# Optimization experiments

Measured on AMD Instinct MI355X. Metric: run time of the kernel, lower is better.

## Reference

```python
import jax, jax.numpy as jnp
import numpy as np

N = 50000          # num_nodes
IN_CH = 128
H = 32             # hidden_channels
D = 2              # stalk dimension d (= final_d, add_lp=add_hp=False)
LAYERS = 4
EU = 400000        # undirected edges
E = 2 * EU         # directed edges (both orientations)
OUT = 32


def setup_inputs() -> dict:
    key = jax.random.key(0)
    ks = jax.random.split(key, 12)
    # undirected random graph; directed edge list holds both orientations so that
    # the reverse of directed edge e is e + EU (mod E)
    u = jax.random.randint(ks[0], (EU,), 0, N)
    v = jax.random.randint(ks[1], (EU,), 0, N)
    edge_index = jnp.stack([jnp.concatenate([u, v]), jnp.concatenate([v, u])]).astype(jnp.int64)
    x = jax.random.normal(ks[2], (N, IN_CH), dtype=jnp.float32)
    W1 = jax.random.normal(ks[3], (H * D, IN_CH), dtype=jnp.float32) / np.sqrt(IN_CH)
    b1 = jax.random.normal(ks[4], (H * D,), dtype=jnp.float32) * 0.01
    W_sheaf = jax.random.normal(ks[5], (LAYERS, D, 2 * D * H), dtype=jnp.float32) / np.sqrt(2 * D * H)
    # lin_left initialised to identity in the module; keep near-identity
    W_left = jnp.tile(jnp.eye(D, dtype=jnp.float32), (LAYERS, 1, 1)) \
        + 0.01 * jax.random.normal(ks[6], (LAYERS, D, D), dtype=jnp.float32)
    W_right = jax.random.normal(ks[7], (LAYERS, H, H), dtype=jnp.float32) / np.sqrt(H)
    eps = jnp.zeros((LAYERS, D, 1), dtype=jnp.float32) + 0.01 * jax.random.normal(ks[8], (LAYERS, D, 1), dtype=jnp.float32)
    W2 = jax.random.normal(ks[9], (OUT, D * H), dtype=jnp.float32) / np.sqrt(D * H)
    b2 = jax.random.normal(ks[10], (OUT,), dtype=jnp.float32) * 0.01
    return {"x": x, "edge_index": edge_index, "W1": W1, "b1": b1, "W_sheaf": W_sheaf,
            "W_left": W_left, "W_right": W_right, "eps": eps, "W2": W2, "b2": b2}


def reference(x, edge_index, W1, b1, W_sheaf, W_left, W_right, eps, W2, b2):
    # eval mode: dropouts are no-ops; diagnostic energies/eigsh omitted (no effect on output)
    n = x.shape[0]
    d = W_left.shape[-1]
    h = W_right.shape[-1]
    src, dst = edge_index[0], edge_index[1]
    e = src.shape[0]
    rev = (jnp.arange(e) + e // 2) % e  # reverse directed edge

    x = jax.nn.elu(x @ W1.T + b1)      # [N, d*h]
    x = x.reshape(n * d, h)
    x0 = x

    for l in range(W_left.shape[0]):
        # --- sheaf learner: tanh(Linear([x_i || x_j])), diag maps F: [E, d] ---
        xn = x.reshape(n, d * h)
        feat = jnp.concatenate([xn[src], xn[dst]], axis=-1)   # [E, 2dh]
        F = jnp.tanh(feat @ W_sheaf[l].T)                     # [E, d]
        Fr = F[rev]
        # --- diag sheaf Laplacian (normalised, augmented: D_hat = D + I) ---
        Dg = jax.ops.segment_sum(F * F, src, num_segments=n)  # [N, d] diagonal blocks
        dinv = jax.lax.rsqrt(Dg + 1.0)
        diagw = Dg * dinv * dinv                              # [N, d]
        offw = -F * Fr * dinv[src] * dinv[dst]                # [E, d]
        # --- left weights: view x^T as [h, N, d], mix stalk dim ---
        xt = x.T.reshape(h, n, d) @ W_left[l].T
        x = xt.reshape(h, n * d).T
        # --- right weights ---
        x = x @ W_right[l].T
        # --- spmm: y = L x ---
        x3 = x.reshape(n, d, h)
        y = diagw[:, :, None] * x3 \
            + jax.ops.segment_sum(offw[:, :, None] * x3[dst], src, num_segments=n)
        x = jax.nn.elu(y.reshape(n * d, h))
        # --- epsilon-gated residual ---
        coeff = jnp.tile(1.0 + jnp.tanh(eps[l]), (n, 1))      # [N*d, 1]
        x0 = coeff * x0 - x
        x = x0

    return x.reshape(n, d * h) @ W2.T + b2
```

## Files before the change

### kernel.cpp

```cpp
#include <hip/hip_runtime.h>
#include <math.h>

#define INCH 128
#define DH 64
#define H  32
#define D  2
#define LAYERS 4
#define OUTC 32

typedef __fp16 half4 __attribute__((ext_vector_type(4)));
typedef float  f32x4 __attribute__((ext_vector_type(4)));

__device__ __forceinline__ float eluf(float v) { return v > 0.f ? v : expm1f(v); }

__device__ __forceinline__ float ftanh(float x) {
    float xc = fminf(9.0f, fmaxf(-9.0f, x));
    float e2 = __builtin_amdgcn_exp2f(xc * 2.885390081777927f);
    return (e2 - 1.0f) * __builtin_amdgcn_rcpf(e2 + 1.0f);
}

__global__ void k_prep(const float* __restrict__ W1, const float* __restrict__ W2,
                       const float* __restrict__ Wleft, const float* __restrict__ Wright,
                       __fp16* __restrict__ W1h, __fp16* __restrict__ W2h,
                       __fp16* __restrict__ Mlrh) {
    int idx = blockIdx.x * blockDim.x + threadIdx.x;
    if (idx < DH * INCH) {
        W1h[idx] = (__fp16)W1[idx];
    } else if (idx < DH * INCH + OUTC * DH) {
        int i = idx - DH * INCH;
        W2h[i] = (__fp16)W2[i];
    } else if (idx < DH * INCH + OUTC * DH + LAYERS * DH * DH) {
        int i = idx - DH * INCH - OUTC * DH;
        int l = i >> 12;
        int r = i & 4095;
        int row = r >> 6;
        int col = r & 63;
        int sp = row >> 5, c = row & 31;
        int s  = col >> 5, cp = col & 31;
        Mlrh[i] = (__fp16)(Wleft[l * 4 + sp * 2 + s] * Wright[l * 1024 + c * 32 + cp]);
    }
}

__global__ void k_hist(const int* __restrict__ src, int* __restrict__ deg, int E) {
    int e = blockIdx.x * blockDim.x + threadIdx.x;
    if (e < E) atomicAdd(&deg[src[e]], 1);
}

__global__ void k_bsum(const int* __restrict__ deg, int* __restrict__ bsum, int N) {
    int b = blockIdx.x, t = threadIdx.x;
    int lane = t & 63, wid = t >> 6;
    int base = b * 1024 + t * 4;
    int s = 0;
    #pragma unroll
    for (int i = 0; i < 4; ++i) {
        int idx = base + i;
        if (idx < N) s += deg[idx];
    }
    #pragma unroll
    for (int ofs = 32; ofs; ofs >>= 1) s += __shfl_xor(s, ofs);
    __shared__ int ws[4];
    if (lane == 0) ws[wid] = s;
    __syncthreads();
    if (t == 0) bsum[b] = ws[0] + ws[1] + ws[2] + ws[3];
}

__global__ void k_scan_small(int* __restrict__ bsum, int B) {
    int lane = threadIdx.x;
    int carry = 0;
    for (int base = 0; base < B; base += 64) {
        int i = base + lane;
        int v = (i < B) ? bsum[i] : 0;
        int incl = v;
        #pragma unroll
        for (int ofs = 1; ofs < 64; ofs <<= 1) {
            int tt = __shfl_up(incl, ofs);
            if (lane >= ofs) incl += tt;
        }
        if (i < B) bsum[i] = carry + incl - v;
        carry += __shfl(incl, 63);
    }
}

__global__ void k_scan_final(const int* __restrict__ deg, const int* __restrict__ bsum,
                             int* __restrict__ rowptr, int* __restrict__ cur, int N) {
    int b = blockIdx.x, t = threadIdx.x;
    int lane = t & 63, wid = t >> 6;
    int base = b * 1024 + t * 4;
    int v[4];
    int s = 0;
    #pragma unroll
    for (int i = 0; i < 4; ++i) {
        int idx = base + i;
        v[i] = (idx < N) ? deg[idx] : 0;
        s += v[i];
    }
    int incl = s;
    #pragma unroll
    for (int ofs = 1; ofs < 64; ofs <<= 1) {
        int tt = __shfl_up(incl, ofs);
        if (lane >= ofs) incl += tt;
    }
    __shared__ int ws[4];
    if (lane == 63) ws[wid] = incl;
    __syncthreads();
    int woff = 0;
    for (int k = 0; k < wid; ++k) woff += ws[k];
    int excl = bsum[b] + woff + incl - s;
    #pragma unroll
    for (int i = 0; i < 4; ++i) {
        int idx = base + i;
        if (idx < N) { rowptr[idx] = excl; cur[idx] = excl; }
        excl += v[i];
        if (idx == N - 1) rowptr[N] = excl;
    }
}

__global__ void k_scatter(const int* __restrict__ src, const int* __restrict__ dst,
                          int* __restrict__ cur, unsigned short* __restrict__ csr_dst, int E) {
    int e = blockIdx.x * blockDim.x + threadIdx.x;
    if (e >= E) return;
    int pos = atomicAdd(&cur[src[e]], 1);
    csr_dst[pos] = (unsigned short)dst[e];
}


__global__ __launch_bounds__(256) void k_mlp1(const float* __restrict__ xin,
                                              const __fp16* __restrict__ W1h,
                                              const float* __restrict__ b1,
                                              float* __restrict__ X, int N) {
    __shared__ float xs[16 * INCH];
    __shared__ __fp16 wsh[DH * 132];
    int t = threadIdx.x;
    int node0 = blockIdx.x * 16;
    for (int i = t; i < 16 * INCH / 4; i += 256) {
        int r = i >> 5, c = (i & 31) * 4;
        int node = node0 + r;
        f32x4 v = (node < N) ? __builtin_nontemporal_load((const f32x4*)(xin + (size_t)node * INCH + c))
                             : (f32x4){0.f, 0.f, 0.f, 0.f};
        *(f32x4*)&xs[r * INCH + c] = v;
    }
    for (int i = t; i < DH * INCH / 4; i += 256) {
        int r = i >> 5, c = (i & 31) * 4;
        *(uint2*)&wsh[r * 132 + c] = ((const uint2*)W1h)[i];
    }
    __syncthreads();
    int w = t >> 6, lane = t & 63;
    int oc0 = w * 16;
    int rr = lane & 15, g = lane >> 4;
    f32x4 acc = {0.f, 0.f, 0.f, 0.f};
    #pragma unroll
    for (int ks = 0; ks < INCH / 16; ++ks) {
        f32x4 xv = *(const f32x4*)&xs[rr * INCH + ks * 16 + g * 4];
        half4 af = {(__fp16)xv.x, (__fp16)xv.y, (__fp16)xv.z, (__fp16)xv.w};
        half4 bf = *(const half4*)&wsh[(oc0 + rr) * 132 + ks * 16 + g * 4];
        acc = __builtin_amdgcn_mfma_f32_16x16x16f16(af, bf, acc, 0, 0, 0);
    }
    int oc = oc0 + rr;
    float bb = b1[oc];
    #pragma unroll
    for (int r = 0; r < 4; ++r) {
        int node = node0 + g * 4 + r;
        if (node < N) X[(size_t)node * DH + oc] = eluf(acc[r] + bb);
    }
}

__global__ void k_pq(const float* __restrict__ X, const float* __restrict__ Wsl,
                     float4* __restrict__ ND8, int N) {
    int wid = (blockIdx.x * blockDim.x + threadIdx.x) >> 6;
    int lane = threadIdx.x & 63;
    if (wid >= N) return;
    float x = X[(size_t)wid * DH + lane];
    float p0 = x * Wsl[lane];
    float q0 = x * Wsl[64 + lane];
    float p1 = x * Wsl[128 + lane];
    float q1 = x * Wsl[192 + lane];
    #pragma unroll
    for (int ofs = 32; ofs; ofs >>= 1) {
        p0 += __shfl_xor(p0, ofs);
        q0 += __shfl_xor(q0, ofs);
        p1 += __shfl_xor(p1, ofs);
        q1 += __shfl_xor(q1, ofs);
    }
    if (lane == 0) ND8[(size_t)wid * 2] = make_float4(p0, p1, q0, q1);
}

__global__ __launch_bounds__(256) void k_lr(const float* __restrict__ X,
                                            const __fp16* __restrict__ Mlrh_l,
                                            __fp16* __restrict__ XW0h,
                                            __fp16* __restrict__ XW1h, int N) {
    __shared__ float xs[16 * DH];
    __shared__ __fp16 mlh[DH * 68];
    int t = threadIdx.x;
    int node0 = blockIdx.x * 16;
    for (int i = t; i < 16 * DH / 4; i += 256) {
        int r = i >> 4, c = (i & 15) * 4;
        int node = node0 + r;
        f32x4 v = (node < N) ? __builtin_nontemporal_load((const f32x4*)(X + (size_t)node * DH + c))
                             : (f32x4){0.f, 0.f, 0.f, 0.f};
        *(f32x4*)&xs[r * DH + c] = v;
    }
    for (int i = t; i < DH * DH / 4; i += 256) {
        int r = i >> 4, c = (i & 15) * 4;
        *(uint2*)&mlh[r * 68 + c] = ((const uint2*)Mlrh_l)[i];
    }
    __syncthreads();
    int w = t >> 6, lane = t & 63;
    int oc0 = w * 16;
    int rr = lane & 15, g = lane >> 4;
    f32x4 acc = {0.f, 0.f, 0.f, 0.f};
    #pragma unroll
    for (int ks = 0; ks < DH / 16; ++ks) {
        f32x4 xv = *(const f32x4*)&xs[rr * DH + ks * 16 + g * 4];
        half4 af = {(__fp16)xv.x, (__fp16)xv.y, (__fp16)xv.z, (__fp16)xv.w};
        half4 bf = *(const half4*)&mlh[(oc0 + rr) * 68 + ks * 16 + g * 4];
        acc = __builtin_amdgcn_mfma_f32_16x16x16f16(af, bf, acc, 0, 0, 0);
    }
    int oc = oc0 + rr;
    int sp = oc >> 5, c = oc & 31;
    __fp16* __restrict__ XWs = sp ? XW1h : XW0h;
    #pragma unroll
    for (int r = 0; r < 4; ++r) {
        int node = node0 + g * 4 + r;
        if (node < N) XWs[(size_t)node * H + c] = (__fp16)acc[r];
    }
}

__global__ __launch_bounds__(256) void k_out(const float* __restrict__ X,
                                             const __fp16* __restrict__ W2h,
                                             const float* __restrict__ b2,
                                             float* __restrict__ out, int N) {
    __shared__ float xs[32 * DH];
    __shared__ __fp16 w2s[OUTC * 68];
    int t = threadIdx.x;
    int node0 = blockIdx.x * 32;
    for (int i = t; i < 32 * DH / 4; i += 256) {
        int r = i >> 4, c = (i & 15) * 4;
        int node = node0 + r;
        f32x4 v = (node < N) ? __builtin_nontemporal_load((const f32x4*)(X + (size_t)node * DH + c))
                             : (f32x4){0.f, 0.f, 0.f, 0.f};
        *(f32x4*)&xs[r * DH + c] = v;
    }
    for (int i = t; i < OUTC * DH / 4; i += 256) {
        int r = i >> 4, c = (i & 15) * 4;
        *(uint2*)&w2s[r * 68 + c] = ((const uint2*)W2h)[i];
    }
    __syncthreads();
    int w = t >> 6, lane = t & 63;
    int nt = w >> 1;
    int oc0 = (w & 1) * 16;
    int rr = lane & 15, g = lane >> 4;
    f32x4 acc = {0.f, 0.f, 0.f, 0.f};
    #pragma unroll
    for (int ks = 0; ks < DH / 16; ++ks) {
        f32x4 xv = *(const f32x4*)&xs[(nt * 16 + rr) * DH + ks * 16 + g * 4];
        half4 af = {(__fp16)xv.x, (__fp16)xv.y, (__fp16)xv.z, (__fp16)xv.w};
        half4 bf = *(const half4*)&w2s[(oc0 + rr) * 68 + ks * 16 + g * 4];
        acc = __builtin_amdgcn_mfma_f32_16x16x16f16(af, bf, acc, 0, 0, 0);
    }
    int oc = oc0 + rr;
    float bb = b2[oc];
    #pragma unroll
    for (int r = 0; r < 4; ++r) {
        int node = node0 + nt * 16 + g * 4 + r;
        if (node < N) out[(size_t)node * OUTC + oc] = acc[r] + bb;
    }
}


__global__ void k_dg(float4* __restrict__ ND8, const int* __restrict__ rowptr,
                     const unsigned short* __restrict__ csr_dst, int N) {
    int wid = (blockIdx.x * blockDim.x + threadIdx.x) >> 6;
    int lane = threadIdx.x & 63;
    int nn = lane >> 4, sub = lane & 15;
    int node = wid * 4 + nn;
    if (node >= N) return;
    float4 pqu = ND8[(size_t)node * 2];
    int pos = rowptr[node], end = rowptr[node + 1];
    float sx = 0.f, sy = 0.f;
    for (int i = pos + sub; i < end; i += 16) {
        int v = (int)__builtin_nontemporal_load(csr_dst + i);
        float4 pqv = ND8[(size_t)v * 2];
        float fx = ftanh(pqu.x + pqv.z);
        float fy = ftanh(pqu.y + pqv.w);
        sx += fx * fx;
        sy += fy * fy;
    }
    #pragma unroll
    for (int ofs = 8; ofs; ofs >>= 1) {
        sx += __shfl_xor(sx, ofs);
        sy += __shfl_xor(sy, ofs);
    }
    if (sub == 0) {
        float i0 = 1.f / (sx + 1.f), i1 = 1.f / (sy + 1.f);
        ND8[(size_t)node * 2 + 1] = make_float4(sqrtf(i0), sqrtf(i1), sx * i0, sy * i1);
    }
}

__global__ void k_spmm_fin_pq(const __fp16* __restrict__ XW0h, const __fp16* __restrict__ XW1h,
                              const float4* __restrict__ ND8, const int* __restrict__ rowptr,
                              const unsigned short* __restrict__ csr_dst,
                              const float* __restrict__ eps_l, const float* __restrict__ Wsn,
                              float* __restrict__ X, float4* __restrict__ ND8n, int N) {
    int wid = (blockIdx.x * blockDim.x + threadIdx.x) >> 6;
    int lane = threadIdx.x & 63;
    if (wid >= N) return;
    int q = lane >> 3;
    int m = lane & 7;
    float4 pqu = ND8[(size_t)wid * 2];
    float4 giu = ND8[(size_t)wid * 2 + 1];
    float dinv0 = giu.x, dinv1 = giu.y;
    int pos = rowptr[wid], end = rowptr[wid + 1];

    float a0x = 0.f, a0y = 0.f, a0z = 0.f, a0w = 0.f;
    float a1x = 0.f, a1y = 0.f, a1z = 0.f, a1w = 0.f;

    for (int chunk = pos; chunk < end; chunk += 64) {
        int myidx = chunk + lane;
        int dmy = 0;
        float w0my = 0.f, w1my = 0.f;
        if (myidx < end) {
            dmy = (int)__builtin_nontemporal_load(csr_dst + myidx);
            float4 pqd = ND8[(size_t)dmy * 2];
            float4 gid = ND8[(size_t)dmy * 2 + 1];
            float ff0 = ftanh(pqu.x + pqd.z), fb0 = ftanh(pqd.x + pqu.z);
            float ff1 = ftanh(pqu.y + pqd.w), fb1 = ftanh(pqd.y + pqu.w);
            w0my = -ff0 * fb0 * dinv0 * gid.x;
            w1my = -ff1 * fb1 * dinv1 * gid.y;
        }
        int lim = end - chunk; if (lim > 64) lim = 64;
        for (int b = 0; b < lim; b += 8) {
            int sl = b + q;
            int d      = __shfl(dmy, sl);
            float w0e  = __shfl(w0my, sl);
            float w1e  = __shfl(w1my, sl);
            half4 g0 = *(const half4*)(XW0h + (size_t)d * H + m * 4);
            half4 g1 = *(const half4*)(XW1h + (size_t)d * H + m * 4);
            a0x += w0e * (float)g0.x; a0y += w0e * (float)g0.y;
            a0z += w0e * (float)g0.z; a0w += w0e * (float)g0.w;
            a1x += w1e * (float)g1.x; a1y += w1e * (float)g1.y;
            a1z += w1e * (float)g1.z; a1w += w1e * (float)g1.w;
        }
    }
    #pragma unroll
    for (int ofs = 8; ofs <= 32; ofs <<= 1) {
        a0x += __shfl_xor(a0x, ofs); a0y += __shfl_xor(a0y, ofs);
        a0z += __shfl_xor(a0z, ofs); a0w += __shfl_xor(a0w, ofs);
        a1x += __shfl_xor(a1x, ofs); a1y += __shfl_xor(a1y, ofs);
        a1z += __shfl_xor(a1z, ofs); a1w += __shfl_xor(a1w, ofs);
    }
    if (q == 0) {
        float diag0 = giu.z;
        float diag1 = giu.w;
        half4 xw0 = *(const half4*)(XW0h + (size_t)wid * H + m * 4);
        half4 xw1 = *(const half4*)(XW1h + (size_t)wid * H + m * 4);
        size_t b0 = (size_t)wid * DH + m * 4;
        size_t b1 = b0 + 32;
        float coeff0 = 1.f + tanhf(eps_l[0]);
        float coeff1 = 1.f + tanhf(eps_l[1]);
        f32x4 xo0 = __builtin_nontemporal_load((const f32x4*)(X + b0));
        f32x4 xo1 = __builtin_nontemporal_load((const f32x4*)(X + b1));
        f32x4 xn0, xn1;
        xn0.x = coeff0 * xo0.x - eluf(diag0 * (float)xw0.x + a0x);
        xn0.y = coeff0 * xo0.y - eluf(diag0 * (float)xw0.y + a0y);
        xn0.z = coeff0 * xo0.z - eluf(diag0 * (float)xw0.z + a0z);
        xn0.w = coeff0 * xo0.w - eluf(diag0 * (float)xw0.w + a0w);
        xn1.x = coeff1 * xo1.x - eluf(diag1 * (float)xw1.x + a1x);
        xn1.y = coeff1 * xo1.y - eluf(diag1 * (float)xw1.y + a1y);
        xn1.z = coeff1 * xo1.z - eluf(diag1 * (float)xw1.z + a1z);
        xn1.w = coeff1 * xo1.w - eluf(diag1 * (float)xw1.w + a1w);
        __builtin_nontemporal_store(xn0, (f32x4*)(X + b0));
        __builtin_nontemporal_store(xn1, (f32x4*)(X + b1));
        if (Wsn) {
            f32x4 wa0 = *(const f32x4*)(Wsn + m * 4);
            f32x4 wa1 = *(const f32x4*)(Wsn + 32 + m * 4);
            f32x4 wb0 = *(const f32x4*)(Wsn + 64 + m * 4);
            f32x4 wb1 = *(const f32x4*)(Wsn + 96 + m * 4);
            f32x4 wc0 = *(const f32x4*)(Wsn + 128 + m * 4);
            f32x4 wc1 = *(const f32x4*)(Wsn + 160 + m * 4);
            f32x4 wd0 = *(const f32x4*)(Wsn + 192 + m * 4);
            f32x4 wd1 = *(const f32x4*)(Wsn + 224 + m * 4);
            float p0 = xn0.x * wa0.x + xn0.y * wa0.y + xn0.z * wa0.z + xn0.w * wa0.w
                     + xn1.x * wa1.x + xn1.y * wa1.y + xn1.z * wa1.z + xn1.w * wa1.w;
            float q0 = xn0.x * wb0.x + xn0.y * wb0.y + xn0.z * wb0.z + xn0.w * wb0.w
                     + xn1.x * wb1.x + xn1.y * wb1.y + xn1.z * wb1.z + xn1.w * wb1.w;
            float p1 = xn0.x * wc0.x + xn0.y * wc0.y + xn0.z * wc0.z + xn0.w * wc0.w
                     + xn1.x * wc1.x + xn1.y * wc1.y + xn1.z * wc1.z + xn1.w * wc1.w;
            float q1 = xn0.x * wd0.x + xn0.y * wd0.y + xn0.z * wd0.z + xn0.w * wd0.w
                     + xn1.x * wd1.x + xn1.y * wd1.y + xn1.z * wd1.z + xn1.w * wd1.w;
            #pragma unroll
            for (int ofs = 1; ofs < 8; ofs <<= 1) {
                p0 += __shfl_xor(p0, ofs);
                q0 += __shfl_xor(q0, ofs);
                p1 += __shfl_xor(p1, ofs);
                q1 += __shfl_xor(q1, ofs);
            }
            if (m == 0) ND8n[(size_t)wid * 2] = make_float4(p0, p1, q0, q1);
        }
    }
}

extern "C" void kernel_launch(void* const* d_in, const int* in_sizes, int n_in,
                              void* d_out, int out_size, void* d_ws, size_t ws_size,
                              hipStream_t stream) {
    const float* xin    = (const float*)d_in[0];
    const int*   ei     = (const int*)d_in[1];
    const float* W1     = (const float*)d_in[2];
    const float* b1     = (const float*)d_in[3];
    const float* Wsheaf = (const float*)d_in[4];
    const float* Wleft  = (const float*)d_in[5];
    const float* Wright = (const float*)d_in[6];
    const float* eps    = (const float*)d_in[7];
    const float* W2     = (const float*)d_in[8];
    const float* b2     = (const float*)d_in[9];
    float* out = (float*)d_out;

    int N = in_sizes[0] / INCH;
    int E = in_sizes[1] / 2;
    const int* src = ei;
    const int* dst = ei + E;

    size_t off = 0;
    auto alloc = [&](size_t nbytes) {
        char* p = (char*)d_ws + off;
        off += (nbytes + 255) & ~(size_t)255;
        return p;
    };
    float*          X       = (float*)alloc((size_t)N * DH * 4);
    __fp16*         XW0h    = (__fp16*)alloc((size_t)N * H * 2);
    __fp16*         XW1h    = (__fp16*)alloc((size_t)N * H * 2);
    float4*         ND8a    = (float4*)alloc((size_t)N * 32);
    float4*         ND8b    = (float4*)alloc((size_t)N * 32);
    int*            deg     = (int*)alloc((size_t)N * 4);
    int*            rowptr  = (int*)alloc(((size_t)N + 1) * 4);
    int*            cur     = (int*)alloc((size_t)N * 4);
    unsigned short* csr_dst = (unsigned short*)alloc((size_t)E * 2);
    int*            bsum    = (int*)alloc(4096);
    __fp16*         W1h     = (__fp16*)alloc((size_t)DH * INCH * 2);
    __fp16*         W2h     = (__fp16*)alloc((size_t)OUTC * DH * 2);
    __fp16*         Mlrh    = (__fp16*)alloc((size_t)LAYERS * DH * DH * 2);

    int B = (N + 1023) / 1024;

    int prep_total = DH * INCH + OUTC * DH + LAYERS * DH * DH;
    k_prep<<<(prep_total + 255) / 256, 256, 0, stream>>>(W1, W2, Wleft, Wright, W1h, W2h, Mlrh);
    hipMemsetAsync(deg, 0, (size_t)N * sizeof(int), stream);
    k_hist<<<(E + 255) / 256, 256, 0, stream>>>(src, deg, E);
    k_bsum<<<B, 256, 0, stream>>>(deg, bsum, N);
    k_scan_small<<<1, 64, 0, stream>>>(bsum, B);
    k_scan_final<<<B, 256, 0, stream>>>(deg, bsum, rowptr, cur, N);
    k_scatter<<<(E + 255) / 256, 256, 0, stream>>>(src, dst, cur, csr_dst, E);

    k_mlp1<<<(N + 15) / 16, 256, 0, stream>>>(xin, W1h, b1, X, N);
    k_pq<<<(N + 3) / 4, 256, 0, stream>>>(X, Wsheaf, ND8a, N);

    float4* NDcur = ND8a;
    float4* NDnext = ND8b;
    for (int l = 0; l < LAYERS; ++l) {
        k_dg<<<(N + 15) / 16, 256, 0, stream>>>(NDcur, rowptr, csr_dst, N);
        k_lr<<<(N + 15) / 16, 256, 0, stream>>>(X, Mlrh + (size_t)l * DH * DH, XW0h, XW1h, N);
        const float* Wsn = (l + 1 < LAYERS) ? (Wsheaf + (l + 1) * 2 * INCH) : nullptr;
        k_spmm_fin_pq<<<(N + 3) / 4, 256, 0, stream>>>(XW0h, XW1h, NDcur, rowptr, csr_dst,
                                                       eps + l * 2, Wsn, X, NDnext, N);
        float4* tmp = NDcur; NDcur = NDnext; NDnext = tmp;
    }

    k_out<<<(N + 31) / 32, 256, 0, stream>>>(X, W2h, b2, out, N);
}
```

Baseline: 402.7 us.

## Fuse pq into mlp1, merge dg and lr launches, store node data as fp16

The first MLP kernel now also computes the sheaf p/q projections from a shared-memory copy of its output, which removes the separate k_pq pass. The degree kernel and the left/right weight kernel are merged into one launch by splitting the grid by block index, so the two independent jobs run side by side and one launch per layer goes away. Per-node sheaf data (p, q, dinv, diag) is packed as eight fp16 values instead of two float4, halving the bytes fetched by the random gathers in the degree and spmm kernels. This costs precision in the tanh arguments and normalisation factors.

Result: faster. 378.4 us (-6.0%).

```diff
diff --git a/kernel.cpp b/kernel.cpp
--- a/kernel.cpp
+++ b/kernel.cpp
@@ -9,6 +9,7 @@
 #define OUTC 32
 
 typedef __fp16 half4 __attribute__((ext_vector_type(4)));
+typedef __fp16 half8 __attribute__((ext_vector_type(8)));
 typedef float  f32x4 __attribute__((ext_vector_type(4)));
 
 __device__ __forceinline__ float eluf(float v) { return v > 0.f ? v : expm1f(v); }
@@ -124,12 +125,15 @@
 }
 
 
-__global__ __launch_bounds__(256) void k_mlp1(const float* __restrict__ xin,
-                                              const __fp16* __restrict__ W1h,
-                                              const float* __restrict__ b1,
-                                              float* __restrict__ X, int N) {
+__global__ __launch_bounds__(256) void k_mlp1_pq(const float* __restrict__ xin,
+                                                 const __fp16* __restrict__ W1h,
+                                                 const float* __restrict__ b1,
+                                                 const float* __restrict__ Ws0,
+                                                 float* __restrict__ X,
+                                                 __fp16* __restrict__ NDh, int N) {
     __shared__ float xs[16 * INCH];
     __shared__ __fp16 wsh[DH * 132];
+    __shared__ float xout[16 * DH];
     int t = threadIdx.x;
     int node0 = blockIdx.x * 16;
     for (int i = t; i < 16 * INCH / 4; i += 256) {
@@ -160,38 +164,77 @@
     #pragma unroll
     for (int r = 0; r < 4; ++r) {
         int node = node0 + g * 4 + r;
-        if (node < N) X[(size_t)node * DH + oc] = eluf(acc[r] + bb);
-    }
-}
-
-__global__ void k_pq(const float* __restrict__ X, const float* __restrict__ Wsl,
-                     float4* __restrict__ ND8, int N) {
-    int wid = (blockIdx.x * blockDim.x + threadIdx.x) >> 6;
-    int lane = threadIdx.x & 63;
-    if (wid >= N) return;
-    float x = X[(size_t)wid * DH + lane];
-    float p0 = x * Wsl[lane];
-    float q0 = x * Wsl[64 + lane];
-    float p1 = x * Wsl[128 + lane];
-    float q1 = x * Wsl[192 + lane];
-    #pragma unroll
-    for (int ofs = 32; ofs; ofs >>= 1) {
-        p0 += __shfl_xor(p0, ofs);
-        q0 += __shfl_xor(q0, ofs);
-        p1 += __shfl_xor(p1, ofs);
-        q1 += __shfl_xor(q1, ofs);
-    }
-    if (lane == 0) ND8[(size_t)wid * 2] = make_float4(p0, p1, q0, q1);
-}
-
-__global__ __launch_bounds__(256) void k_lr(const float* __restrict__ X,
-                                            const __fp16* __restrict__ Mlrh_l,
-                                            __fp16* __restrict__ XW0h,
-                                            __fp16* __restrict__ XW1h, int N) {
+        float v = eluf(acc[r] + bb);
+        xout[(g * 4 + r) * DH + oc] = v;
+        if (node < N) X[(size_t)node * DH + oc] = v;
+    }
+    __syncthreads();
+    float wsa = Ws0[lane];
+    float wsb = Ws0[64 + lane];
+    float wsc = Ws0[128 + lane];
+    float wsd = Ws0[192 + lane];
+    #pragma unroll
+    for (int j = 0; j < 4; ++j) {
+        int nl = w * 4 + j;
+        int node = node0 + nl;
+        float x = xout[nl * DH + lane];
+        float p0 = x * wsa, q0 = x * wsb, p1 = x * wsc, q1 = x * wsd;
+        #pragma unroll
+        for (int ofs = 32; ofs; ofs >>= 1) {
+            p0 += __shfl_xor(p0, ofs);
+            q0 += __shfl_xor(q0, ofs);
+            p1 += __shfl_xor(p1, ofs);
+            q1 += __shfl_xor(q1, ofs);
+        }
+        if (lane == 0 && node < N) {
+            half4 pq = {(__fp16)p0, (__fp16)p1, (__fp16)q0, (__fp16)q1};
+            *(half4*)(NDh + (size_t)node * 8) = pq;
+        }
+    }
+}
+
+__global__ __launch_bounds__(256) void k_dglr(__fp16* __restrict__ NDh,
+                                              const int* __restrict__ rowptr,
+                                              const unsigned short* __restrict__ csr_dst,
+                                              const float* __restrict__ X,
+                                              const __fp16* __restrict__ Mlrh_l,
+                                              __fp16* __restrict__ XW0h,
+                                              __fp16* __restrict__ XW1h,
+                                              int Bdg, int N) {
     __shared__ float xs[16 * DH];
     __shared__ __fp16 mlh[DH * 68];
+    if (blockIdx.x < Bdg) {
+        int lane = threadIdx.x & 63;
+        int widl = threadIdx.x >> 6;
+        int nn = lane >> 4, sub = lane & 15;
+        int node = blockIdx.x * 16 + widl * 4 + nn;
+        if (node >= N) return;
+        half4 pqu = *(const half4*)(NDh + (size_t)node * 8);
+        float pu0 = (float)pqu[0], pu1 = (float)pqu[1];
+        int pos = rowptr[node], end = rowptr[node + 1];
+        float sx = 0.f, sy = 0.f;
+        for (int i = pos + sub; i < end; i += 16) {
+            int v = (int)__builtin_nontemporal_load(csr_dst + i);
+            half4 pqv = *(const half4*)(NDh + (size_t)v * 8);
+            float fx = ftanh(pu0 + (float)pqv[2]);
+            float fy = ftanh(pu1 + (float)pqv[3]);
+            sx += fx * fx;
+            sy += fy * fy;
+        }
+        #pragma unroll
+        for (int ofs = 8; ofs; ofs >>= 1) {
+            sx += __shfl_xor(sx, ofs);
+            sy += __shfl_xor(sy, ofs);
+        }
+        if (sub == 0) {
+            float i0 = 1.f / (sx + 1.f), i1 = 1.f / (sy + 1.f);
+            half4 gi = {(__fp16)sqrtf(i0), (__fp16)sqrtf(i1), (__fp16)(sx * i0), (__fp16)(sy * i1)};
+            *(half4*)(NDh + (size_t)node * 8 + 4) = gi;
+        }
+        return;
+    }
     int t = threadIdx.x;
-    int node0 = blockIdx.x * 16;
+    int node0 = (blockIdx.x - Bdg) * 16;
     for (int i = t; i < 16 * DH / 4; i += 256) {
         int r = i >> 4, c = (i & 15) * 4;
         int node = node0 + r;
@@ -266,49 +309,20 @@
     }
 }
 
-
-__global__ void k_dg(float4* __restrict__ ND8, const int* __restrict__ rowptr,
-                     const unsigned short* __restrict__ csr_dst, int N) {
-    int wid = (blockIdx.x * blockDim.x + threadIdx.x) >> 6;
-    int lane = threadIdx.x & 63;
-    int nn = lane >> 4, sub = lane & 15;
-    int node = wid * 4 + nn;
-    if (node >= N) return;
-    float4 pqu = ND8[(size_t)node * 2];
-    int pos = rowptr[node], end = rowptr[node + 1];
-    float sx = 0.f, sy = 0.f;
-    for (int i = pos + sub; i < end; i += 16) {
-        int v = (int)__builtin_nontemporal_load(csr_dst + i);
-        float4 pqv = ND8[(size_t)v * 2];
-        float fx = ftanh(pqu.x + pqv.z);
-        float fy = ftanh(pqu.y + pqv.w);
-        sx += fx * fx;
-        sy += fy * fy;
-    }
-    #pragma unroll
-    for (int ofs = 8; ofs; ofs >>= 1) {
-        sx += __shfl_xor(sx, ofs);
-        sy += __shfl_xor(sy, ofs);
-    }
-    if (sub == 0) {
-        float i0 = 1.f / (sx + 1.f), i1 = 1.f / (sy + 1.f);
-        ND8[(size_t)node * 2 + 1] = make_float4(sqrtf(i0), sqrtf(i1), sx * i0, sy * i1);
-    }
-}
-
 __global__ void k_spmm_fin_pq(const __fp16* __restrict__ XW0h, const __fp16* __restrict__ XW1h,
-                              const float4* __restrict__ ND8, const int* __restrict__ rowptr,
+                              const __fp16* __restrict__ NDh, const int* __restrict__ rowptr,
                               const unsigned short* __restrict__ csr_dst,
                               const float* __restrict__ eps_l, const float* __restrict__ Wsn,
-                              float* __restrict__ X, float4* __restrict__ ND8n, int N) {
+                              float* __restrict__ X, __fp16* __restrict__ NDhn, int N) {
     int wid = (blockIdx.x * blockDim.x + threadIdx.x) >> 6;
     int lane = threadIdx.x & 63;
     if (wid >= N) return;
     int q = lane >> 3;
     int m = lane & 7;
-    float4 pqu = ND8[(size_t)wid * 2];
-    float4 giu = ND8[(size_t)wid * 2 + 1];
-    float dinv0 = giu.x, dinv1 = giu.y;
+    half8 ndu = *(const half8*)(NDh + (size_t)wid * 8);
+    float pu0 = (float)ndu[0], pu1 = (float)ndu[1];
+    float qu0 = (float)ndu[2], qu1 = (float)ndu[3];
+    float dinv0 = (float)ndu[4], dinv1 = (float)ndu[5];
     int pos = rowptr[wid], end = rowptr[wid + 1];
 
     float a0x = 0.f, a0y = 0.f, a0z = 0.f, a0w = 0.f;
@@ -320,12 +334,11 @@
         float w0my = 0.f, w1my = 0.f;
         if (myidx < end) {
             dmy = (int)__builtin_nontemporal_load(csr_dst + myidx);
-            float4 pqd = ND8[(size_t)dmy * 2];
-            float4 gid = ND8[(size_t)dmy * 2 + 1];
-            float ff0 = ftanh(pqu.x + pqd.z), fb0 = ftanh(pqd.x + pqu.z);
-            float ff1 = ftanh(pqu.y + pqd.w), fb1 = ftanh(pqd.y + pqu.w);
-            w0my = -ff0 * fb0 * dinv0 * gid.x;
-            w1my = -ff1 * fb1 * dinv1 * gid.y;
+            half8 ndd = *(const half8*)(NDh + (size_t)dmy * 8);
+            float ff0 = ftanh(pu0 + (float)ndd[2]), fb0 = ftanh((float)ndd[0] + qu0);
+            float ff1 = ftanh(pu1 + (float)ndd[3]), fb1 = ftanh((float)ndd[1] + qu1);
+            w0my = -ff0 * fb0 * dinv0 * (float)ndd[4];
+            w1my = -ff1 * fb1 * dinv1 * (float)ndd[5];
         }
         int lim = end - chunk; if (lim > 64) lim = 64;
         for (int b = 0; b < lim; b += 8) {
@@ -349,8 +362,8 @@
         a1z += __shfl_xor(a1z, ofs); a1w += __shfl_xor(a1w, ofs);
     }
     if (q == 0) {
-        float diag0 = giu.z;
-        float diag1 = giu.w;
+        float diag0 = (float)ndu[6];
+        float diag1 = (float)ndu[7];
         half4 xw0 = *(const half4*)(XW0h + (size_t)wid * H + m * 4);
         half4 xw1 = *(const half4*)(XW1h + (size_t)wid * H + m * 4);
         size_t b0 = (size_t)wid * DH + m * 4;
@@ -394,7 +407,10 @@
                 p1 += __shfl_xor(p1, ofs);
                 q1 += __shfl_xor(q1, ofs);
             }
-            if (m == 0) ND8n[(size_t)wid * 2] = make_float4(p0, p1, q0, q1);
+            if (m == 0) {
+                half4 pq = {(__fp16)p0, (__fp16)p1, (__fp16)q0, (__fp16)q1};
+                *(half4*)(NDhn + (size_t)wid * 8) = pq;
+            }
         }
     }
 }
@@ -428,8 +444,8 @@
     float*          X       = (float*)alloc((size_t)N * DH * 4);
     __fp16*         XW0h    = (__fp16*)alloc((size_t)N * H * 2);
     __fp16*         XW1h    = (__fp16*)alloc((size_t)N * H * 2);
-    float4*         ND8a    = (float4*)alloc((size_t)N * 32);
-    float4*         ND8b    = (float4*)alloc((size_t)N * 32);
+    __fp16*         NDha    = (__fp16*)alloc((size_t)N * 16);
+    __fp16*         NDhb    = (__fp16*)alloc((size_t)N * 16);
     int*            deg     = (int*)alloc((size_t)N * 4);
     int*            rowptr  = (int*)alloc(((size_t)N + 1) * 4);
     int*            cur     = (int*)alloc((size_t)N * 4);
@@ -450,18 +466,19 @@
     k_scan_final<<<B, 256, 0, stream>>>(deg, bsum, rowptr, cur, N);
     k_scatter<<<(E + 255) / 256, 256, 0, stream>>>(src, dst, cur, csr_dst, E);
 
-    k_mlp1<<<(N + 15) / 16, 256, 0, stream>>>(xin, W1h, b1, X, N);
-    k_pq<<<(N + 3) / 4, 256, 0, stream>>>(X, Wsheaf, ND8a, N);
-
-    float4* NDcur = ND8a;
-    float4* NDnext = ND8b;
+    k_mlp1_pq<<<(N + 15) / 16, 256, 0, stream>>>(xin, W1h, b1, Wsheaf, X, NDha, N);
+
+    __fp16* NDcur = NDha;
+    __fp16* NDnext = NDhb;
+    int Bdg = (N + 15) / 16;
+    int Blr = (N + 15) / 16;
     for (int l = 0; l < LAYERS; ++l) {
-        k_dg<<<(N + 15) / 16, 256, 0, stream>>>(NDcur, rowptr, csr_dst, N);
-        k_lr<<<(N + 15) / 16, 256, 0, stream>>>(X, Mlrh + (size_t)l * DH * DH, XW0h, XW1h, N);
+        k_dglr<<<Bdg + Blr, 256, 0, stream>>>(NDcur, rowptr, csr_dst, X,
+                                              Mlrh + (size_t)l * DH * DH, XW0h, XW1h, Bdg, N);
         const float* Wsn = (l + 1 < LAYERS) ? (Wsheaf + (l + 1) * 2 * INCH) : nullptr;
         k_spmm_fin_pq<<<(N + 3) / 4, 256, 0, stream>>>(XW0h, XW1h, NDcur, rowptr, csr_dst,
                                                        eps + l * 2, Wsn, X, NDnext, N);
-        float4* tmp = NDcur; NDcur = NDnext; NDnext = tmp;
+        __fp16* tmp = NDcur; NDcur = NDnext; NDnext = tmp;
     }
 
     k_out<<<(N + 31) / 32, 256, 0, stream>>>(X, W2h, b2, out, N);
```
